# Kernel tuning notes

Measured on AMD Instinct MI355X. Metric: run time of the kernel, lower is better.

The kernel has to match this reference:

```python
import jax, jax.numpy as jnp
import numpy as np

N_NODES = 100000

def _sage_conv(h, src, dst, Wl, bl, Wr):
    # PyG SAGEConv (mean aggr): out = lin_l(mean_{j in N(i)} h_j) + lin_r(h_i)
    msg = h[src]                                            # [E, H] gather
    agg = jax.ops.segment_sum(msg, dst, num_segments=N_NODES)   # [N, H] scatter-add
    cnt = jax.ops.segment_sum(jnp.ones((src.shape[0],), h.dtype), dst, num_segments=N_NODES)
    mean = agg / jnp.maximum(cnt, 1.0)[:, None]
    return mean @ Wl + bl + h @ Wr

def setup_inputs() -> dict:
    key = jax.random.key(0)
    ks = jax.random.split(key, 12)
    IN, H, C, E = 256, 128, 40, 1600000
    s = 0.05
    return {
        "x": jax.random.normal(ks[0], (N_NODES, IN), jnp.float32),
        "edge_index": jax.random.randint(ks[1], (2, E), 0, N_NODES, jnp.int32),
        "W_pre": jax.random.normal(ks[2], (IN, H), jnp.float32) * s,
        "b_pre": jnp.zeros((H,), jnp.float32),
        "Wl0": jax.random.normal(ks[3], (H, H), jnp.float32) * s,
        "bl0": jnp.zeros((H,), jnp.float32),
        "Wr0": jax.random.normal(ks[4], (H, H), jnp.float32) * s,
        "Wl1": jax.random.normal(ks[5], (H, H), jnp.float32) * s,
        "bl1": jnp.zeros((H,), jnp.float32),
        "Wr1": jax.random.normal(ks[6], (H, H), jnp.float32) * s,
        "W_post": jax.random.normal(ks[7], (H, C), jnp.float32) * s,
        "b_post": jnp.zeros((C,), jnp.float32),
    }

def reference(x, edge_index, W_pre, b_pre, Wl0, bl0, Wr0, Wl1, bl1, Wr1, W_post, b_post):
    src, dst = edge_index[0], edge_index[1]
    h = x @ W_pre + b_pre                       # pre Linear
    # two SAGEConv layers + relu (dropout is identity in eval mode)
    h = jax.nn.relu(_sage_conv(h, src, dst, Wl0, bl0, Wr0))
    h = jax.nn.relu(_sage_conv(h, src, dst, Wl1, bl1, Wr1))
    logits = h @ W_post + b_post                # post Linear
    return jax.nn.log_softmax(logits, axis=1)
```

## Files before the change

kernel.cpp:

```cpp
#include <hip/hip_runtime.h>
#include <hip/hip_bf16.h>
#include <math.h>

#define N_NODES 100000
#define IN_F 256
#define HID 128
#define NCLS 40

#define NB 782
#define BN 128
#define NC 448
#define CSZ2 3584

typedef __attribute__((ext_vector_type(8))) short short8;
typedef __attribute__((ext_vector_type(4))) float f32x4;

__device__ __forceinline__ short f2bf(float f){
  union { float f; unsigned u; } x; x.f = f;
  unsigned r = (x.u + 0x7fffu + ((x.u >> 16) & 1u)) >> 16;
  return (short)r;
}
__device__ __forceinline__ float bf2f(unsigned short u){
  union { unsigned u; float f; } x; x.u = ((unsigned)u) << 16;
  return x.f;
}
__device__ __forceinline__ unsigned char f2i8(float v){
  float q = fmaf(v, 16.f, 128.5f);
  q = fminf(fmaxf(q, 0.f), 255.f);
  return (unsigned char)q;
}

__global__ __launch_bounds__(256) void k_wprep(
    const float* __restrict__ Wpre, const float* __restrict__ Wl0,
    const float* __restrict__ Wr0,  const float* __restrict__ Wl1,
    const float* __restrict__ Wr1,  const float* __restrict__ Wpost,
    unsigned short* __restrict__ img)
{
  const int g = blockIdx.x*256 + threadIdx.x;
  if(g >= 13056) return;
  const int base = g*8;
  unsigned short v[8];
  if(base < 98304){
    const int which = base >> 15;
    const int idx = base & 32767;
    const int l = (idx >> 3) & 63, kb = (idx >> 9) & 7, ct = idx >> 12;
    const int col = ct*16 + (l & 15);
    const float* Wsrc; int kbase;
    if(which == 0){ Wsrc = Wpre; kbase = kb*32 + (l>>4)*8; }
    else{
      Wsrc = (which==1) ? ((kb<4) ? Wl0 : Wr0) : ((kb<4) ? Wl1 : Wr1);
      kbase = (kb&3)*32 + (l>>4)*8;
    }
    #pragma unroll
    for(int j = 0; j < 8; j++) v[j] = (unsigned short)f2bf(Wsrc[(size_t)(kbase+j)*HID + col]);
  } else {
    const int idx = base - 98304;
    const int l = (idx >> 3) & 63, kb = (idx >> 9) & 3, ct = idx >> 11;
    const int col = ct*16 + (l & 15);
    const int kbase = kb*32 + (l>>4)*8;
    #pragma unroll
    for(int j = 0; j < 8; j++)
      v[j] = (col < NCLS) ? (unsigned short)f2bf(Wpost[(size_t)(kbase+j)*NCLS + col]) : 0;
  }
  *reinterpret_cast<short8*>(img + base) = *reinterpret_cast<const short8*>(v);
}

__global__ __launch_bounds__(256) void k_hist(const int* __restrict__ dst, int E,
                                              int* __restrict__ cnt){
  __shared__ int hist[NB];
  const int c = blockIdx.x;
  for(int i = threadIdx.x; i < NB; i += 256) hist[i] = 0;
  __syncthreads();
  const int s0 = c*CSZ2, s1 = min(s0 + CSZ2, E);
  for(int i = s0 + threadIdx.x; i < s1; i += 256)
    atomicAdd(&hist[(unsigned)__builtin_nontemporal_load(dst + i) >> 7], 1);
  __syncthreads();
  for(int i = threadIdx.x; i < NB; i += 256) cnt[c*NB + i] = hist[i];
}

__global__ __launch_bounds__(256) void k_bscanA(const int* __restrict__ cnt,
                                                int* __restrict__ wbase,
                                                int* __restrict__ btot){
  __shared__ int s[256];
  const int b = blockIdx.x;
  const int t = threadIdx.x;
  int v0 = 0, v1 = 0;
  if(2*t < NC)     v0 = cnt[(2*t)*NB + b];
  if(2*t + 1 < NC) v1 = cnt[(2*t+1)*NB + b];
  s[t] = v0 + v1; __syncthreads();
  for(int d = 1; d < 256; d <<= 1){
    int add = (t >= d) ? s[t-d] : 0;
    __syncthreads();
    s[t] += add;
    __syncthreads();
  }
  const int ex = (t > 0) ? s[t-1] : 0;
  if(2*t < NC)     wbase[(2*t)*NB + b] = ex;
  if(2*t + 1 < NC) wbase[(2*t+1)*NB + b] = ex + v0;
  if(t == 255) btot[b] = s[255];
}

__global__ __launch_bounds__(1024) void k_bscanB(const int* __restrict__ btot,
                                                 int* __restrict__ bstart, int E){
  __shared__ int s[1024];
  const int t = threadIdx.x;
  int v = (t < NB) ? btot[t] : 0;
  s[t] = v; __syncthreads();
  for(int d = 1; d < 1024; d <<= 1){
    int add = (t >= d) ? s[t-d] : 0;
    __syncthreads();
    s[t] += add;
    __syncthreads();
  }
  if(t < NB) bstart[t] = s[t] - v;
  if(t == 0) bstart[NB] = E;
}

__global__ __launch_bounds__(256) void k_place(const int* __restrict__ src,
                                               const int* __restrict__ dst, int E,
                                               const int* __restrict__ wbase,
                                               const int* __restrict__ bstart,
                                               int* __restrict__ pk){
  const int g = blockIdx.x;
  const int c = (g & 7)*(NC/8) + (g >> 3);
  __shared__ int cur[NB];
  for(int i = threadIdx.x; i < NB; i += 256)
    cur[i] = wbase[c*NB + i] + bstart[i];
  __syncthreads();
  const int s0 = c*CSZ2, s1 = min(s0 + CSZ2, E);
  for(int i = s0 + threadIdx.x; i < s1; i += 256){
    const int d  = __builtin_nontemporal_load(dst + i);
    const int sv = __builtin_nontemporal_load(src + i);
    const int pos = atomicAdd(&cur[(unsigned)d >> 7], 1);
    pk[pos] = ((d & 127) << 17) | sv;
  }
}

__global__ __launch_bounds__(512) void k_sortb(const int* __restrict__ pk,
                                               const int* __restrict__ bstart,
                                               int* __restrict__ esrc2,
                                               int* __restrict__ nodeoff, int E){
  __shared__ int hist[BN];
  __shared__ int nofs[BN];
  __shared__ int curs[BN];
  const int b = blockIdx.x;
  const int t = threadIdx.x;
  const int bs = bstart[b];
  const int ne = bstart[b+1] - bs;
  for(int i = t; i < BN; i += 512) hist[i] = 0;
  __syncthreads();
  for(int i = t; i < ne; i += 512)
    atomicAdd(&hist[(unsigned)pk[bs + i] >> 17], 1);
  __syncthreads();
  if(t < BN) nofs[t] = hist[t];
  __syncthreads();
  for(int d = 1; d < BN; d <<= 1){
    int add = 0;
    if(t < BN && t >= d) add = nofs[t-d];
    __syncthreads();
    if(t < BN) nofs[t] += add;
    __syncthreads();
  }
  if(t < BN){
    curs[t] = nofs[t] - hist[t];
    const int node = b*BN + t;
    if(node < N_NODES) nodeoff[node] = bs + nofs[t] - hist[t];
    if(node == N_NODES - 1 || (b == NB-1 && t == BN-1)) nodeoff[N_NODES] = E;
  }
  __syncthreads();
  for(int i = t; i < ne; i += 512){
    const int e = pk[bs + i];
    const int pos = atomicAdd(&curs[(unsigned)e >> 17], 1);
    esrc2[bs + pos] = e & 0x1ffff;
  }
}

__global__ __launch_bounds__(256) void k_agg3(
    const unsigned short* __restrict__ h, const int* __restrict__ nodeoff,
    const int* __restrict__ esrc2, unsigned short* __restrict__ mean)
{
  const int lane = threadIdx.x & 63;
  const int wid = blockIdx.x*4 + (threadIdx.x >> 6);
  const int wstride = gridDim.x*4;
  const unsigned* hp = (const unsigned*)h;
  for(int node = wid; node < N_NODES; node += wstride){
    const int beg = nodeoff[node];
    const int deg = nodeoff[node+1] - beg;
    float a0 = 0.f, a1 = 0.f;
    for(int base = 0; base < deg; base += 64){
      const int rem = deg - base;
      const int cnt = rem < 64 ? rem : 64;
      const int myi = (lane < cnt) ? esrc2[beg + base + lane] : 0;
      int e = 0;
      for(; e + 8 <= cnt; e += 8){
        unsigned v[8];
        #pragma unroll
        for(int u = 0; u < 8; u++){
          const int s = __builtin_amdgcn_readlane(myi, e + u);
          v[u] = hp[(size_t)s*64 + lane];
        }
        #pragma unroll
        for(int u = 0; u < 8; u++){
          a0 += bf2f((unsigned short)(v[u] & 0xffffu));
          a1 += bf2f((unsigned short)(v[u] >> 16));
        }
      }
      for(; e < cnt; e++){
        const int s = __builtin_amdgcn_readlane(myi, e);
        const unsigned vv = hp[(size_t)s*64 + lane];
        a0 += bf2f((unsigned short)(vv & 0xffffu));
        a1 += bf2f((unsigned short)(vv >> 16));
      }
    }
    const float inv = (deg > 0) ? (1.0f/(float)deg) : 0.f;
    a0 *= inv; a1 *= inv;
    const unsigned o = ((unsigned)(unsigned short)f2bf(a1) << 16) | (unsigned)(unsigned short)f2bf(a0);
    ((unsigned*)mean)[(size_t)node*64 + lane] = o;
  }
}

__global__ __launch_bounds__(256) void k_agg8(
    const unsigned char* __restrict__ h8, const int* __restrict__ nodeoff,
    const int* __restrict__ esrc2, unsigned short* __restrict__ mean)
{
  const int lane = threadIdx.x & 63;
  const int wid = blockIdx.x*4 + (threadIdx.x >> 6);
  const int wstride = gridDim.x*4;
  const unsigned short* hp = (const unsigned short*)h8;
  for(int node = wid; node < N_NODES; node += wstride){
    const int beg = nodeoff[node];
    const int deg = nodeoff[node+1] - beg;
    float a0 = 0.f, a1 = 0.f;
    for(int base = 0; base < deg; base += 64){
      const int rem = deg - base;
      const int cnt = rem < 64 ? rem : 64;
      const int myi = (lane < cnt) ? esrc2[beg + base + lane] : 0;
      int e = 0;
      for(; e + 8 <= cnt; e += 8){
        unsigned short v[8];
        #pragma unroll
        for(int u = 0; u < 8; u++)
          v[u] = hp[(size_t)__builtin_amdgcn_readlane(myi, e + u)*64 + lane];
        #pragma unroll
        for(int u = 0; u < 8; u++){
          a0 += (float)(v[u] & 0xffu);
          a1 += (float)(v[u] >> 8);
        }
      }
      for(; e < cnt; e++){
        const unsigned short vv = hp[(size_t)__builtin_amdgcn_readlane(myi, e)*64 + lane];
        a0 += (float)(vv & 0xffu);
        a1 += (float)(vv >> 8);
      }
    }
    float m0 = 0.f, m1 = 0.f;
    if(deg > 0){
      const float inv = 1.0f/(float)deg;
      m0 = (a0*inv - 128.f)*0.0625f;
      m1 = (a1*inv - 128.f)*0.0625f;
    }
    const unsigned o = ((unsigned)(unsigned short)f2bf(m1) << 16) | (unsigned)(unsigned short)f2bf(m0);
    ((unsigned*)mean)[(size_t)node*64 + lane] = o;
  }
}

__global__ __launch_bounds__(256) void k_gemm_pre(
    const float* __restrict__ x, const unsigned short* __restrict__ wimg,
    const float* __restrict__ b, unsigned short* __restrict__ out,
    unsigned char* __restrict__ h8)
{
  const int t = threadIdx.x;
  const int wave = t >> 6, lane = t & 63;
  const int r_in = lane & 15, kg = lane >> 4;
  const int tile = blockIdx.x*4 + wave;
  if(tile >= N_NODES/16) return;
  const int row0 = tile*16;
  const float* xp = x + (size_t)(row0 + r_in)*IN_F + kg*8;

  float4 xa0[4], xb0[4], xa1[4], xb1[4];
  #pragma unroll
  for(int kb = 0; kb < 4; kb++){
    xa0[kb] = *reinterpret_cast<const float4*>(xp + kb*32);
    xb0[kb] = *reinterpret_cast<const float4*>(xp + kb*32 + 4);
  }
  #pragma unroll
  for(int kb = 0; kb < 4; kb++){
    xa1[kb] = *reinterpret_cast<const float4*>(xp + (kb+4)*32);
    xb1[kb] = *reinterpret_cast<const float4*>(xp + (kb+4)*32 + 4);
  }
  f32x4 acc[8];
  #pragma unroll
  for(int ct = 0; ct < 8; ct++) acc[ct] = (f32x4){0.f,0.f,0.f,0.f};
  #pragma unroll
  for(int kb = 0; kb < 4; kb++){
    short8 a;
    a[0]=f2bf(xa0[kb].x); a[1]=f2bf(xa0[kb].y); a[2]=f2bf(xa0[kb].z); a[3]=f2bf(xa0[kb].w);
    a[4]=f2bf(xb0[kb].x); a[5]=f2bf(xb0[kb].y); a[6]=f2bf(xb0[kb].z); a[7]=f2bf(xb0[kb].w);
    #pragma unroll
    for(int ct = 0; ct < 8; ct++){
      short8 bb = *reinterpret_cast<const short8*>(wimg + ((ct*8+kb)*64+lane)*8);
      acc[ct] = __builtin_amdgcn_mfma_f32_16x16x32_bf16(a, bb, acc[ct], 0, 0, 0);
    }
  }
  #pragma unroll
  for(int kb = 4; kb < 8; kb++){
    short8 a;
    a[0]=f2bf(xa1[kb-4].x); a[1]=f2bf(xa1[kb-4].y); a[2]=f2bf(xa1[kb-4].z); a[3]=f2bf(xa1[kb-4].w);
    a[4]=f2bf(xb1[kb-4].x); a[5]=f2bf(xb1[kb-4].y); a[6]=f2bf(xb1[kb-4].z); a[7]=f2bf(xb1[kb-4].w);
    #pragma unroll
    for(int ct = 0; ct < 8; ct++){
      short8 bb = *reinterpret_cast<const short8*>(wimg + ((ct*8+kb)*64+lane)*8);
      acc[ct] = __builtin_amdgcn_mfma_f32_16x16x32_bf16(a, bb, acc[ct], 0, 0, 0);
    }
  }
  #pragma unroll
  for(int ct = 0; ct < 8; ct++){
    const int col = ct*16 + r_in;
    const float bias = b[col];
    #pragma unroll
    for(int i = 0; i < 4; i++){
      const int row = row0 + kg*4 + i;
      const float v = acc[ct][i] + bias;
      out[(size_t)row*HID + col] = (unsigned short)f2bf(v);
      if(h8) h8[(size_t)row*HID + col] = f2i8(v);
    }
  }
}

__global__ __launch_bounds__(256) void k_gemm_sage(
    const unsigned short* __restrict__ mean, const unsigned short* __restrict__ h,
    const unsigned short* __restrict__ wimg, const float* __restrict__ bl,
    unsigned short* __restrict__ out, unsigned char* __restrict__ h8out)
{
  __shared__ short wlds[8*8*64*8];
  const int t = threadIdx.x;
  {
    short8* dstp = reinterpret_cast<short8*>(wlds);
    const short8* srcp = reinterpret_cast<const short8*>(wimg);
    #pragma unroll
    for(int i = 0; i < 16; i++) dstp[t + i*256] = srcp[t + i*256];
  }
  __syncthreads();
  const int wave = t >> 6, lane = t & 63;
  const int r_in = lane & 15, kg = lane >> 4;
  const int NT = N_NODES/16, stride = gridDim.x*4;

  auto loadx = [&](int tile, short8 (&am)[4], short8 (&ah)[4]){
    const size_t base = (size_t)(tile*16 + r_in)*HID + kg*8;
    #pragma unroll
    for(int kb = 0; kb < 4; kb++){
      am[kb] = *reinterpret_cast<const short8*>(mean + base + kb*32);
      ah[kb] = *reinterpret_cast<const short8*>(h    + base + kb*32);
    }
  };
  auto compute = [&](int tile, const short8 (&am)[4], const short8 (&ah)[4]){
    f32x4 acc[8];
    #pragma unroll
    for(int ct = 0; ct < 8; ct++) acc[ct] = (f32x4){0.f,0.f,0.f,0.f};
    #pragma unroll
    for(int kb = 0; kb < 8; kb++){
      short8 a = (kb < 4) ? am[kb & 3] : ah[kb & 3];
      #pragma unroll
      for(int ct = 0; ct < 8; ct++){
        short8 bb = *reinterpret_cast<const short8*>(&wlds[((ct*8+kb)*64+lane)*8]);
        acc[ct] = __builtin_amdgcn_mfma_f32_16x16x32_bf16(a, bb, acc[ct], 0, 0, 0);
      }
    }
    const int row0 = tile*16;
    #pragma unroll
    for(int ct = 0; ct < 8; ct++){
      const int col = ct*16 + r_in;
      const float bias = bl[col];
      #pragma unroll
      for(int i = 0; i < 4; i++){
        const int row = row0 + kg*4 + i;
        float v = fmaxf(acc[ct][i] + bias, 0.f);
        out[(size_t)row*HID + col] = (unsigned short)f2bf(v);
        if(h8out) h8out[(size_t)row*HID + col] = f2i8(v);
      }
    }
  };

  int tile = blockIdx.x*4 + wave;
  if(tile >= NT) return;
  short8 amA[4], ahA[4], amB[4], ahB[4];
  loadx(tile, amA, ahA);
  for(;;){
    int nt = tile + stride;
    bool more = nt < NT;
    if(more) loadx(nt, amB, ahB);
    compute(tile, amA, ahA);
    if(!more) break;
    tile = nt;
    nt = tile + stride;
    more = nt < NT;
    if(more) loadx(nt, amA, ahA);
    compute(tile, amB, ahB);
    if(!more) break;
    tile = nt;
  }
}

__global__ __launch_bounds__(256) void k_post(
    const unsigned short* __restrict__ h, const unsigned short* __restrict__ wimg,
    const float* __restrict__ b, float* __restrict__ out)
{
  __shared__ short wlds[3*4*64*8];
  __shared__ float bias_s[48];
  const int t = threadIdx.x;
  {
    short8* dstp = reinterpret_cast<short8*>(wlds);
    const short8* srcp = reinterpret_cast<const short8*>(wimg);
    for(int i = t; i < 768; i += 256) dstp[i] = srcp[i];
  }
  if(t < 48) bias_s[t] = (t < NCLS) ? b[t] : -1e30f;
  __syncthreads();
  const int wave = t >> 6, lane = t & 63;
  const int r_in = lane & 15, kg = lane >> 4;
  for(int tile = blockIdx.x*4 + wave; tile < N_NODES/16; tile += gridDim.x*4){
    const int row0 = tile*16;
    f32x4 acc[3];
    #pragma unroll
    for(int ct = 0; ct < 3; ct++) acc[ct] = (f32x4){0.f,0.f,0.f,0.f};
    #pragma unroll
    for(int kb = 0; kb < 4; kb++){
      short8 a = *reinterpret_cast<const short8*>(h + (size_t)(row0 + r_in)*HID + kb*32 + kg*8);
      #pragma unroll
      for(int ct = 0; ct < 3; ct++){
        short8 bb = *reinterpret_cast<const short8*>(&wlds[((ct*4+kb)*64+lane)*8]);
        acc[ct] = __builtin_amdgcn_mfma_f32_16x16x32_bf16(a, bb, acc[ct], 0, 0, 0);
      }
    }
    #pragma unroll
    for(int i = 0; i < 4; i++){
      float v0 = acc[0][i] + bias_s[r_in];
      float v1 = acc[1][i] + bias_s[16 + r_in];
      float v2 = acc[2][i] + bias_s[32 + r_in];
      float m = fmaxf(fmaxf(v0, v1), v2);
      #pragma unroll
      for(int o = 8; o > 0; o >>= 1) m = fmaxf(m, __shfl_xor(m, o));
      float s = expf(v0 - m) + expf(v1 - m) + expf(v2 - m);
      #pragma unroll
      for(int o = 8; o > 0; o >>= 1) s += __shfl_xor(s, o);
      const float ls = m + logf(s);
      const int row = row0 + kg*4 + i;
      float* op = out + (size_t)row*NCLS;
      op[r_in] = v0 - ls;
      op[16 + r_in] = v1 - ls;
      if(r_in < 8) op[32 + r_in] = v2 - ls;
    }
  }
}

extern "C" void kernel_launch(void* const* d_in, const int* in_sizes, int n_in,
                              void* d_out, int out_size, void* d_ws, size_t ws_size,
                              hipStream_t stream)
{
  const float* x      = (const float*)d_in[0];
  const int*   ei     = (const int*)  d_in[1];
  const float* W_pre  = (const float*)d_in[2];
  const float* b_pre  = (const float*)d_in[3];
  const float* Wl0    = (const float*)d_in[4];
  const float* bl0    = (const float*)d_in[5];
  const float* Wr0    = (const float*)d_in[6];
  const float* Wl1    = (const float*)d_in[7];
  const float* bl1    = (const float*)d_in[8];
  const float* Wr1    = (const float*)d_in[9];
  const float* W_post = (const float*)d_in[10];
  const float* b_post = (const float*)d_in[11];
  float* out = (float*)d_out;

  const int E = in_sizes[1] / 2;
  const int* src = ei;
  const int* dst = ei + E;

  char* ws = (char*)d_ws;
  size_t off = 0;
  auto alloc = [&](size_t bytes)->void*{
    void* p = ws + off;
    off += (bytes + 255) & ~(size_t)255;
    return p;
  };
  unsigned short* hA = (unsigned short*)alloc((size_t)N_NODES*HID*2);
  unsigned short* hB = (unsigned short*)alloc((size_t)N_NODES*HID*2);
  unsigned short* hM = (unsigned short*)alloc((size_t)N_NODES*HID*2);
  int* pk      = (int*)alloc((size_t)E*4);
  int* esrc2   = (int*)alloc((size_t)E*4);
  int* cnt     = (int*)alloc((size_t)NC*NB*4);
  int* wbase   = (int*)alloc((size_t)NC*NB*4);
  int* btot    = (int*)alloc((size_t)NB*4);
  int* bstart  = (int*)alloc((size_t)(NB+1)*4);
  int* nodeoff = (int*)alloc((size_t)(N_NODES+1)*4);
  unsigned short* wimg = (unsigned short*)alloc(104448*2);
  unsigned char* h8A = (unsigned char*)alloc((size_t)N_NODES*HID);
  unsigned char* h8B = (unsigned char*)alloc((size_t)N_NODES*HID);
  const bool use8 = (off <= ws_size);

  k_wprep<<<51, 256, 0, stream>>>(W_pre, Wl0, Wr0, Wl1, Wr1, W_post, wimg);

  k_hist<<<NC, 256, 0, stream>>>(dst, E, cnt);
  k_bscanA<<<NB, 256, 0, stream>>>(cnt, wbase, btot);
  k_bscanB<<<1, 1024, 0, stream>>>(btot, bstart, E);
  k_place<<<NC, 256, 0, stream>>>(src, dst, E, wbase, bstart, pk);
  k_sortb<<<NB, 512, 0, stream>>>(pk, bstart, esrc2, nodeoff, E);

  k_gemm_pre<<<1563, 256, 0, stream>>>(x, wimg, b_pre, hA, use8 ? h8A : nullptr);

  if(use8){
    k_agg8<<<4096, 256, 0, stream>>>(h8A, nodeoff, esrc2, hM);
    k_gemm_sage<<<512, 256, 0, stream>>>(hM, hA, wimg + 32768, bl0, hB, h8B);
    k_agg8<<<4096, 256, 0, stream>>>(h8B, nodeoff, esrc2, hM);
    k_gemm_sage<<<512, 256, 0, stream>>>(hM, hB, wimg + 65536, bl1, hA, nullptr);
  } else {
    k_agg3<<<4096, 256, 0, stream>>>(hA, nodeoff, esrc2, hM);
    k_gemm_sage<<<512, 256, 0, stream>>>(hM, hA, wimg + 32768, bl0, hB, nullptr);
    k_agg3<<<4096, 256, 0, stream>>>(hB, nodeoff, esrc2, hM);
    k_gemm_sage<<<512, 256, 0, stream>>>(hM, hB, wimg + 65536, bl1, hA, nullptr);
  }

  k_post<<<1563, 256, 0, stream>>>(hA, wimg + 98304, b_post, out);
}
```

Before: 249.7 us.

## Pre-convert input features to bf16 and use persistent double-buffered pre-GEMM

Adds a pass that converts x from fp32 to bf16 into workspace. A new persistent pre-linear GEMM kernel caches the weight tile in LDS and double-buffers bf16 row tiles across a grid-stride loop. The aim is to cut per-block weight reloads and overlap loads with MFMA compute. In exchange, the extra conversion pass writes and rereads a bf16 copy of x, adding memory traffic. It also needs enough workspace, otherwise the old path is used.

```diff
diff --git a/kernel.cpp b/kernel.cpp
--- a/kernel.cpp
+++ b/kernel.cpp
@@ -28,6 +28,20 @@
   float q = fmaf(v, 16.f, 128.5f);
   q = fminf(fmaxf(q, 0.f), 255.f);
   return (unsigned char)q;
+}
+
+__global__ __launch_bounds__(256) void k_xconv(const float* __restrict__ x,
+                                               unsigned short* __restrict__ xbf, int n8){
+  int i = blockIdx.x*256 + threadIdx.x;
+  const int stride = gridDim.x*256;
+  for(; i < n8; i += stride){
+    const float4 a = *reinterpret_cast<const float4*>(x + (size_t)i*8);
+    const float4 b = *reinterpret_cast<const float4*>(x + (size_t)i*8 + 4);
+    short8 v;
+    v[0]=f2bf(a.x); v[1]=f2bf(a.y); v[2]=f2bf(a.z); v[3]=f2bf(a.w);
+    v[4]=f2bf(b.x); v[5]=f2bf(b.y); v[6]=f2bf(b.z); v[7]=f2bf(b.w);
+    *reinterpret_cast<short8*>(xbf + (size_t)i*8) = v;
+  }
 }
 
 __global__ __launch_bounds__(256) void k_wprep(
@@ -264,6 +278,77 @@
   }
 }
 
+__global__ __launch_bounds__(256) void k_gemm_pre_bf(
+    const unsigned short* __restrict__ xbf, const unsigned short* __restrict__ wimg,
+    const float* __restrict__ b, unsigned short* __restrict__ out,
+    unsigned char* __restrict__ h8)
+{
+  __shared__ short wlds[8*8*64*8];
+  const int t = threadIdx.x;
+  {
+    short8* dstp = reinterpret_cast<short8*>(wlds);
+    const short8* srcp = reinterpret_cast<const short8*>(wimg);
+    #pragma unroll
+    for(int i = 0; i < 16; i++) dstp[t + i*256] = srcp[t + i*256];
+  }
+  __syncthreads();
+  const int wave = t >> 6, lane = t & 63;
+  const int r_in = lane & 15, kg = lane >> 4;
+  const int NT = N_NODES/16, stride = gridDim.x*4;
+
+  auto loadx = [&](int tile, short8 (&a)[8]){
+    const size_t base = (size_t)(tile*16 + r_in)*IN_F + kg*8;
+    #pragma unroll
+    for(int kb = 0; kb < 8; kb++)
+      a[kb] = *reinterpret_cast<const short8*>(xbf + base + kb*32);
+  };
+  auto compute = [&](int tile, const short8 (&av)[8]){
+    f32x4 acc[8];
+    #pragma unroll
+    for(int ct = 0; ct < 8; ct++) acc[ct] = (f32x4){0.f,0.f,0.f,0.f};
+    #pragma unroll
+    for(int kb = 0; kb < 8; kb++){
+      #pragma unroll
+      for(int ct = 0; ct < 8; ct++){
+        short8 bb = *reinterpret_cast<const short8*>(&wlds[((ct*8+kb)*64+lane)*8]);
+        acc[ct] = __builtin_amdgcn_mfma_f32_16x16x32_bf16(av[kb], bb, acc[ct], 0, 0, 0);
+      }
+    }
+    const int row0 = tile*16;
+    #pragma unroll
+    for(int ct = 0; ct < 8; ct++){
+      const int col = ct*16 + r_in;
+      const float bias = b[col];
+      #pragma unroll
+      for(int i = 0; i < 4; i++){
+        const int row = row0 + kg*4 + i;
+        const float v = acc[ct][i] + bias;
+        out[(size_t)row*HID + col] = (unsigned short)f2bf(v);
+        if(h8) h8[(size_t)row*HID + col] = f2i8(v);
+      }
+    }
+  };
+
+  int tile = blockIdx.x*4 + wave;
+  if(tile >= NT) return;
+  short8 aA[8], aB[8];
+  loadx(tile, aA);
+  for(;;){
+    int nt = tile + stride;
+    bool more = nt < NT;
+    if(more) loadx(nt, aB);
+    compute(tile, aA);
+    if(!more) break;
+    tile = nt;
+    nt = tile + stride;
+    more = nt < NT;
+    if(more) loadx(nt, aA);
+    compute(tile, aB);
+    if(!more) break;
+    tile = nt;
+  }
+}
+
 __global__ __launch_bounds__(256) void k_gemm_pre(
     const float* __restrict__ x, const unsigned short* __restrict__ wimg,
     const float* __restrict__ b, unsigned short* __restrict__ out,
@@ -495,6 +580,8 @@
   unsigned char* h8A = (unsigned char*)alloc((size_t)N_NODES*HID);
   unsigned char* h8B = (unsigned char*)alloc((size_t)N_NODES*HID);
   const bool use8 = (off <= ws_size);
+  unsigned short* xbf = (unsigned short*)alloc((size_t)N_NODES*IN_F*2);
+  const bool useXbf = (off <= ws_size);
 
   k_wprep<<<51, 256, 0, stream>>>(W_pre, Wl0, Wr0, Wl1, Wr1, W_post, wimg);
 
@@ -504,7 +591,12 @@
   k_place<<<NC, 256, 0, stream>>>(src, dst, E, wbase, bstart, pk);
   k_sortb<<<NB, 512, 0, stream>>>(pk, bstart, esrc2, nodeoff, E);
 
-  k_gemm_pre<<<1563, 256, 0, stream>>>(x, wimg, b_pre, hA, use8 ? h8A : nullptr);
+  if(useXbf){
+    k_xconv<<<2048, 256, 0, stream>>>(x, xbf, N_NODES*IN_F/8);
+    k_gemm_pre_bf<<<512, 256, 0, stream>>>(xbf, wimg, b_pre, hA, use8 ? h8A : nullptr);
+  } else {
+    k_gemm_pre<<<1563, 256, 0, stream>>>(x, wimg, b_pre, hA, use8 ? h8A : nullptr);
+  }
 
   if(use8){
     k_agg8<<<4096, 256, 0, stream>>>(h8A, nodeoff, esrc2, hM);
```

After: 266.3 us. 6.6% more time.
